# Performance work log

Hardware: AMD Instinct MI355X
Metric: run time of the kernel (lower is better)

## Reference

```python
import jax, jax.numpy as jnp
import numpy as np

N = 100000
E = 1600000
IN, HID, OUT = 128, 256, 47


def _glorot(key, shape):
    fan_in, fan_out = shape
    lim = np.sqrt(6.0 / (fan_in + fan_out))
    return jax.random.uniform(key, shape, jnp.float32, -lim, lim)


def setup_inputs() -> dict:
    key = jax.random.key(0)
    ks = jax.random.split(key, 12)
    x = jax.random.normal(ks[0], (N, IN), jnp.float32)
    src = jax.random.randint(ks[1], (E,), 0, N, jnp.int32)
    dst = jax.random.randint(ks[2], (E,), 0, N, jnp.int32)
    dims = [(IN, HID), (HID, HID), (HID, OUT)]
    inp = {"x": x, "src": src, "dst": dst}
    for i, (di, do) in enumerate(dims, 1):
        inp[f"w_self{i}"] = _glorot(ks[2 + 3 * i - 2], (di, do))
        inp[f"w_neigh{i}"] = _glorot(ks[2 + 3 * i - 1], (di, do))
        inp[f"b{i}"] = jnp.zeros((do,), jnp.float32)
    return inp


def sage_conv(x, src, dst, w_self, w_neigh, b):
    n = x.shape[0]
    msg = x[src]                                              # [E, d] gather
    summed = jax.ops.segment_sum(msg, dst, num_segments=n)    # [N, d]
    deg = jax.ops.segment_sum(jnp.ones((src.shape[0],), x.dtype), dst, num_segments=n)
    h_neigh = summed / jnp.maximum(deg, 1.0)[:, None]         # mean aggregate
    return x @ w_self + h_neigh @ w_neigh + b


def reference(x, src, dst, w_self1, w_neigh1, b1, w_self2, w_neigh2, b2, w_self3, w_neigh3, b3):
    h = sage_conv(x, src, dst, w_self1, w_neigh1, b1)
    h = jax.nn.relu(h)  # dropout = identity in eval mode
    h = sage_conv(h, src, dst, w_self2, w_neigh2, b2)
    h = jax.nn.relu(h)
    h = sage_conv(h, src, dst, w_self3, w_neigh3, b3)
    return h
```

## Files before the change

kernel.cpp:

```cpp
#include <hip/hip_runtime.h>

#define N_NODES 100000
#define N_EDGES 1600000

typedef __attribute__((ext_vector_type(8))) _Float16 half8;
typedef __attribute__((ext_vector_type(4))) _Float16 half4v;
typedef __attribute__((ext_vector_type(4))) float floatx4;


__global__ void deg_rank(const int* __restrict__ dst, int* __restrict__ deg,
                         int* __restrict__ rank, int e) {
    int i = blockIdx.x * blockDim.x + threadIdx.x;
    if (i < e) rank[i] = atomicAdd(&deg[dst[i]], 1);
}


__global__ __launch_bounds__(256) void scan_partial(const int* __restrict__ deg,
                                                    int* __restrict__ bsum, int n) {
    __shared__ int wsum[4];
    int t = threadIdx.x;
    int base = blockIdx.x * 2048 + t * 8;
    int tsum = 0;
    #pragma unroll
    for (int k = 0; k < 8; ++k) {
        int idx = base + k;
        tsum += (idx < n) ? deg[idx] : 0;
    }
    #pragma unroll
    for (int d = 1; d < 64; d <<= 1) tsum += __shfl_xor(tsum, d, 64);
    if ((t & 63) == 0) wsum[t >> 6] = tsum;
    __syncthreads();
    if (t == 0) bsum[blockIdx.x] = wsum[0] + wsum[1] + wsum[2] + wsum[3];
}

__global__ void scan_blocksums(const int* __restrict__ bsum, int* __restrict__ bbase, int nb) {
    int t = threadIdx.x;
    int v = (t < nb) ? bsum[t] : 0;
    int s = v;
    #pragma unroll
    for (int d = 1; d < 64; d <<= 1) {
        int u = __shfl_up(s, d, 64);
        if (t >= d) s += u;
    }
    if (t < nb) bbase[t] = s - v;
    if (t == 63) bbase[nb] = s;
}

__global__ __launch_bounds__(256) void scan_write(const int* __restrict__ deg,
                                                  const int* __restrict__ bbase,
                                                  int* __restrict__ offs, int n, int nb) {
    __shared__ int wsum[4];
    int t = threadIdx.x;
    int lane = t & 63, w = t >> 6;
    int base = blockIdx.x * 2048 + t * 8;
    int v[8];
    #pragma unroll
    for (int k = 0; k < 8; ++k) {
        int idx = base + k;
        v[k] = (idx < n) ? deg[idx] : 0;
    }
    int tsum = 0;
    #pragma unroll
    for (int k = 0; k < 8; ++k) { int x = v[k]; v[k] = tsum; tsum += x; }
    int s = tsum;
    #pragma unroll
    for (int d = 1; d < 64; d <<= 1) {
        int u = __shfl_up(s, d, 64);
        if (lane >= d) s += u;
    }
    if (lane == 63) wsum[w] = s;
    __syncthreads();
    int wb = 0;
    for (int j = 0; j < w; ++j) wb += wsum[j];
    int texcl = bbase[blockIdx.x] + wb + (s - tsum);
    #pragma unroll
    for (int k = 0; k < 8; ++k) {
        int idx = base + k;
        if (idx < n) offs[idx] = texcl + v[k];
    }
    if (blockIdx.x == 0 && t == 0) offs[n] = bbase[nb];
}

__global__ void fill_csr2(const int* __restrict__ src, const int* __restrict__ dst,
                          const int* __restrict__ offs, const int* __restrict__ rank,
                          int* __restrict__ csr, int e) {
    int i = blockIdx.x * blockDim.x + threadIdx.x;
    if (i < e) csr[offs[dst[i]] + rank[i]] = src[i];
}


__global__ void cvt_f16(const float4* __restrict__ in, half4v* __restrict__ oh, int n4) {
    int i = blockIdx.x * blockDim.x + threadIdx.x;
    if (i >= n4) return;
    float4 v = in[i];
    half4v h;
    h[0] = (_Float16)v.x; h[1] = (_Float16)v.y;
    h[2] = (_Float16)v.z; h[3] = (_Float16)v.w;
    oh[i] = h;
}


__global__ void prep_all(const float* __restrict__ ws1, const float* __restrict__ wn1,
                         const float* __restrict__ ws2, const float* __restrict__ wn2,
                         const float* __restrict__ ws3, const float* __restrict__ wn3,
                         _Float16* __restrict__ o1s, _Float16* __restrict__ o1n,
                         _Float16* __restrict__ o2s, _Float16* __restrict__ o2n,
                         _Float16* __restrict__ o3c) {
    int i = blockIdx.x * blockDim.x + threadIdx.x;
    if (i < 65536) {
        const float* W = (i < 32768) ? ws1 : wn1;
        _Float16* O = (i < 32768) ? o1s : o1n;
        int j = i & 32767;
        int nn = j >> 7, k = j & 127;
        O[j] = (_Float16)W[k * 256 + nn];
    } else if (i < 196608) {
        int j = i - 65536;
        const float* W = (j < 65536) ? ws2 : wn2;
        _Float16* O = (j < 65536) ? o2s : o2n;
        j &= 65535;
        int nn = j >> 8, k = j & 255;
        O[j] = (_Float16)W[k * 256 + nn];
    } else if (i < 221184) {
        int j = i - 196608;
        const float* W = (j < 12288) ? ws3 : wn3;
        _Float16* O = o3c + ((j < 12288) ? 0 : 12288);
        j = (j < 12288) ? j : j - 12288;
        int nn = j >> 8, k = j & 255;
        O[j] = (nn < 47) ? (_Float16)W[k * 47 + nn] : (_Float16)0.f;
    }
}


__global__ __launch_bounds__(256) void aggP(const _Float16* __restrict__ Xp,
                                            const int* __restrict__ csr,
                                            const int* __restrict__ offs,
                                            _Float16* __restrict__ Pp, int n) {
    int node = blockIdx.x * 4 + (threadIdx.x >> 6);
    int lane = threadIdx.x & 63;
    int qtr = lane >> 4;
    int sl = lane & 15;
    if (node >= n) return;
    int e0 = offs[node], e1 = offs[node + 1];
    float a[8] = {0.f, 0.f, 0.f, 0.f, 0.f, 0.f, 0.f, 0.f};
    int e = e0;
    for (; e + 16 <= e1; e += 16) {
        int s0 = csr[e + qtr];
        int s1 = csr[e + 4 + qtr];
        int s2 = csr[e + 8 + qtr];
        int s3 = csr[e + 12 + qtr];
        half8 u0 = ((const half8*)(Xp + (size_t)s0 * 128))[sl];
        half8 u1 = ((const half8*)(Xp + (size_t)s1 * 128))[sl];
        half8 u2 = ((const half8*)(Xp + (size_t)s2 * 128))[sl];
        half8 u3 = ((const half8*)(Xp + (size_t)s3 * 128))[sl];
        #pragma unroll
        for (int j = 0; j < 8; ++j) a[j] += (float)u0[j];
        #pragma unroll
        for (int j = 0; j < 8; ++j) a[j] += (float)u1[j];
        #pragma unroll
        for (int j = 0; j < 8; ++j) a[j] += (float)u2[j];
        #pragma unroll
        for (int j = 0; j < 8; ++j) a[j] += (float)u3[j];
    }
    for (; e + 8 <= e1; e += 8) {
        int s0 = csr[e + qtr];
        int s1 = csr[e + 4 + qtr];
        half8 u0 = ((const half8*)(Xp + (size_t)s0 * 128))[sl];
        half8 u1 = ((const half8*)(Xp + (size_t)s1 * 128))[sl];
        #pragma unroll
        for (int j = 0; j < 8; ++j) a[j] += (float)u0[j];
        #pragma unroll
        for (int j = 0; j < 8; ++j) a[j] += (float)u1[j];
    }
    for (; e + 4 <= e1; e += 4) {
        int s = csr[e + qtr];
        half8 u = ((const half8*)(Xp + (size_t)s * 128))[sl];
        #pragma unroll
        for (int j = 0; j < 8; ++j) a[j] += (float)u[j];
    }
    int rem = e1 - e;
    if (qtr < rem) {
        int s = csr[e + qtr];
        half8 u = ((const half8*)(Xp + (size_t)s * 128))[sl];
        #pragma unroll
        for (int j = 0; j < 8; ++j) a[j] += (float)u[j];
    }
    #pragma unroll
    for (int j = 0; j < 8; ++j) {
        a[j] += __shfl_xor(a[j], 16);
        a[j] += __shfl_xor(a[j], 32);
    }
    if (lane < 16) {
        float inv = 1.0f / fmaxf((float)(e1 - e0), 1.0f);
        half8 rh;
        #pragma unroll
        for (int j = 0; j < 8; ++j) rh[j] = (_Float16)(a[j] * inv);
        ((half8*)(Pp + (size_t)node * 128))[sl] = rh;
    }
}

__global__ __launch_bounds__(256) void agg_l3(const _Float16* __restrict__ Y,
                                              const float* __restrict__ S,
                                              const int* __restrict__ csr,
                                              const int* __restrict__ offs,
                                              float* __restrict__ out, int n) {
    int node = blockIdx.x * 4 + (threadIdx.x >> 6);
    int lane = threadIdx.x & 63;
    int qtr = lane >> 4;
    int sl = lane & 15;
    int c = sl < 12 ? sl : 11;
    if (node >= n) return;
    int e0 = offs[node], e1 = offs[node + 1];
    float a0 = 0.f, a1 = 0.f, a2 = 0.f, a3 = 0.f;
    int e = e0;
    for (; e + 8 <= e1; e += 8) {
        int s0 = csr[e + qtr];
        int s1 = csr[e + 4 + qtr];
        half4v f0 = ((const half4v*)(Y + (size_t)s0 * 48))[c];
        half4v f1 = ((const half4v*)(Y + (size_t)s1 * 48))[c];
        a0 += (float)f0[0] + (float)f1[0];
        a1 += (float)f0[1] + (float)f1[1];
        a2 += (float)f0[2] + (float)f1[2];
        a3 += (float)f0[3] + (float)f1[3];
    }
    for (; e + 4 <= e1; e += 4) {
        int s = csr[e + qtr];
        half4v f = ((const half4v*)(Y + (size_t)s * 48))[c];
        a0 += (float)f[0]; a1 += (float)f[1]; a2 += (float)f[2]; a3 += (float)f[3];
    }
    int rem = e1 - e;
    if (qtr < rem) {
        int s = csr[e + qtr];
        half4v f = ((const half4v*)(Y + (size_t)s * 48))[c];
        a0 += (float)f[0]; a1 += (float)f[1]; a2 += (float)f[2]; a3 += (float)f[3];
    }
    a0 += __shfl_xor(a0, 16); a0 += __shfl_xor(a0, 32);
    a1 += __shfl_xor(a1, 16); a1 += __shfl_xor(a1, 32);
    a2 += __shfl_xor(a2, 16); a2 += __shfl_xor(a2, 32);
    a3 += __shfl_xor(a3, 16); a3 += __shfl_xor(a3, 32);
    if (lane < 12) {
        float inv = 1.0f / fmaxf((float)(e1 - e0), 1.0f);
        float4 sv = ((const float4*)(S + (size_t)node * 48))[c];
        float r[4] = {sv.x + a0 * inv, sv.y + a1 * inv, sv.z + a2 * inv, sv.w + a3 * inv};
        #pragma unroll
        for (int k = 0; k < 4; ++k) {
            int col = c * 4 + k;
            if (col < 47) out[(size_t)node * 47 + col] = r[k];
        }
    }
}


template <int NTILES, int OUTFMT>
__global__ __launch_bounds__(256, 2) void gemm_mfma(
    const _Float16* __restrict__ A1h, const _Float16* __restrict__ A2h,
    const _Float16* __restrict__ W1, const _Float16* __restrict__ W2,
    const float* __restrict__ bias, float* __restrict__ outS, _Float16* __restrict__ outY,
    _Float16* __restrict__ outh, int n, int K, int dout, int relu, int phases) {
    constexpr int NPAD = NTILES * 16;
    constexpr int LDT = 36;
    __shared__ _Float16 Bs[NPAD * LDT];

    const int t = threadIdx.x;
    const int bm = blockIdx.x * 128;
    const int lane = t & 63;
    const int w = t >> 6;
    const int quad = lane >> 4;
    const int tl = lane & 15;
    const int r0 = bm + w * 32 + tl;
    const int r1 = r0 + 16;
    const size_t PS = (size_t)n * 128;

    floatx4 acc[2][NTILES];
    #pragma unroll
    for (int i = 0; i < 2; ++i)
        #pragma unroll
        for (int j = 0; j < NTILES; ++j) acc[i][j] = (floatx4){0.f, 0.f, 0.f, 0.f};

    const int spp = K >> 5;
    const int nsteps = phases * spp;

    half8 pb0, pb1, pb2, pb3;
    half8 pah0 = {0}, pah1 = {0};

    if (t < NPAD) {
        const half8* p = (const half8*)(W1 + (size_t)t * K);
        pb0 = p[0]; pb1 = p[1]; pb2 = p[2]; pb3 = p[3];
    }
    {
        int kq = quad * 8;
        if (r0 < n) pah0 = *(const half8*)(A1h + (size_t)r0 * 128 + kq);
        if (r1 < n) pah1 = *(const half8*)(A1h + (size_t)r1 * 128 + kq);
    }

    for (int s = 0; s < nsteps; ++s) {
        __syncthreads();
        if (t < NPAD) {
            *(half8*)&Bs[t * LDT + 0]  = pb0;
            *(half8*)&Bs[t * LDT + 8]  = pb1;
            *(half8*)&Bs[t * LDT + 16] = pb2;
            *(half8*)&Bs[t * LDT + 24] = pb3;
        }
        __syncthreads();
        half8 ah0 = pah0, ah1 = pah1;
        if (s + 1 < nsteps) {
            int s2 = s + 1;
            int ph2 = (s2 >= spp) ? 1 : 0;
            int k02 = (ph2 ? s2 - spp : s2) << 5;
            if (t < NPAD) {
                const _Float16* W = ph2 ? W2 : W1;
                const half8* p = (const half8*)(W + (size_t)t * K + k02);
                pb0 = p[0]; pb1 = p[1]; pb2 = p[2]; pb3 = p[3];
            }
            const _Float16* Ah = ph2 ? A2h : A1h;
            int kq = k02 + quad * 8;
            const _Float16* Ab = Ah + ((kq >> 7) ? PS : (size_t)0) + (kq & 127);
            pah0 = (half8){0}; pah1 = (half8){0};
            if (r0 < n) pah0 = *(const half8*)(Ab + (size_t)r0 * 128);
            if (r1 < n) pah1 = *(const half8*)(Ab + (size_t)r1 * 128);
        }
        #pragma unroll
        for (int nt = 0; nt < NTILES; ++nt) {
            half8 bh = *(const half8*)&Bs[(nt * 16 + tl) * LDT + quad * 8];
            acc[0][nt] = __builtin_amdgcn_mfma_f32_16x16x32_f16(ah0, bh, acc[0][nt], 0, 0, 0);
            acc[1][nt] = __builtin_amdgcn_mfma_f32_16x16x32_f16(ah1, bh, acc[1][nt], 0, 0, 0);
        }
    }

    #pragma unroll
    for (int mt = 0; mt < 2; ++mt) {
        #pragma unroll
        for (int nt = 0; nt < NTILES; ++nt) {
            int gc = nt * 16 + tl;
            if (OUTFMT == 1 && gc >= dout) continue;
            #pragma unroll
            for (int r = 0; r < 4; ++r) {
                int gr = bm + w * 32 + mt * 16 + quad * 4 + r;
                if (gr >= n) continue;
                float v = acc[mt][nt][r];
                if (OUTFMT == 1) {
                    v += bias[gc];
                    if (relu) v = fmaxf(v, 0.f);
                    outh[(size_t)(gc >> 7) * PS + (size_t)gr * 128 + (gc & 127)] = (_Float16)v;
                } else {
                    if (gc < 48) {
                        v += (gc < 47) ? bias[gc] : 0.f;
                        outS[(size_t)gr * 48 + gc] = v;
                    } else {
                        outY[(size_t)gr * 48 + (gc - 48)] = (_Float16)v;
                    }
                }
            }
        }
    }
}

extern "C" void kernel_launch(void* const* d_in, const int* in_sizes, int n_in,
                              void* d_out, int out_size, void* d_ws, size_t ws_size,
                              hipStream_t stream) {
    (void)in_sizes; (void)n_in; (void)out_size; (void)ws_size;
    const int N = N_NODES, E = N_EDGES;
    const float* x = (const float*)d_in[0];
    const int* src = (const int*)d_in[1];
    const int* dst = (const int*)d_in[2];
    const float* w_self1 = (const float*)d_in[3];
    const float* w_neigh1 = (const float*)d_in[4];
    const float* b1 = (const float*)d_in[5];
    const float* w_self2 = (const float*)d_in[6];
    const float* w_neigh2 = (const float*)d_in[7];
    const float* b2 = (const float*)d_in[8];
    const float* w_self3 = (const float*)d_in[9];
    const float* w_neigh3 = (const float*)d_in[10];
    const float* b3 = (const float*)d_in[11];
    float* out = (float*)d_out;

    _Float16* Ph = (_Float16*)d_ws;
    _Float16* Hh = Ph + (size_t)N * 256;
    int* deg = (int*)(Hh + (size_t)N * 256);
    int* offs = deg + N;
    int* csr = offs + N + 4;
    _Float16* wbuf = (_Float16*)(csr + E);
    _Float16* w1s = wbuf;
    _Float16* w1n = w1s + 32768;
    _Float16* w2s = w1n + 32768;
    _Float16* w2n = w2s + 65536;
    _Float16* w3c = w2n + 65536;
    int* bsum = (int*)(w3c + 24576);
    int* bbase = bsum + 64;
    int* rank = (int*)Ph;
    _Float16* xh = Ph + (size_t)N * 128;
    float* S = (float*)Ph;
    _Float16* Y = (_Float16*)(S + (size_t)N * 48);

    const int NB = (N + 2047) / 2048;

    hipMemsetAsync(deg, 0, N * sizeof(int), stream);
    deg_rank<<<(E + 255) / 256, 256, 0, stream>>>(dst, deg, rank, E);
    scan_partial<<<NB, 256, 0, stream>>>(deg, bsum, N);
    scan_blocksums<<<1, 64, 0, stream>>>(bsum, bbase, NB);
    scan_write<<<NB, 256, 0, stream>>>(deg, bbase, offs, N, NB);
    fill_csr2<<<(E + 255) / 256, 256, 0, stream>>>(src, dst, offs, rank, csr, E);

    cvt_f16<<<(N * 128 / 4 + 255) / 256, 256, 0, stream>>>((const float4*)x, (half4v*)xh,
                                                           N * 128 / 4);
    prep_all<<<(221184 + 255) / 256, 256, 0, stream>>>(w_self1, w_neigh1, w_self2, w_neigh2,
                                                       w_self3, w_neigh3, w1s, w1n, w2s, w2n,
                                                       w3c);

    int gemmGrid = (N + 127) / 128;
    int aggGrid = (N + 3) / 4;

    aggP<<<aggGrid, 256, 0, stream>>>(xh, csr, offs, Ph, N);
    gemm_mfma<16, 1><<<gemmGrid, 256, 0, stream>>>(xh, Ph, w1s, w1n, b1, nullptr, nullptr,
                                                   Hh, N, 128, 256, 1, 2);
    aggP<<<aggGrid, 256, 0, stream>>>(Hh, csr, offs, Ph, N);
    aggP<<<aggGrid, 256, 0, stream>>>(Hh + (size_t)N * 128, csr, offs, Ph + (size_t)N * 128, N);
    gemm_mfma<16, 1><<<gemmGrid, 256, 0, stream>>>(Hh, Ph, w2s, w2n, b2, nullptr, nullptr,
                                                   Hh, N, 256, 256, 1, 2);
    gemm_mfma<6, 2><<<gemmGrid, 256, 0, stream>>>(Hh, nullptr, w3c, nullptr, b3, S, Y,
                                                  nullptr, N, 256, 96, 0, 1);
    agg_l3<<<aggGrid, 256, 0, stream>>>(Y, S, csr, offs, out, N);
}
```

Measured before the change: 641.5 us.

## Load GEMM weights directly from global into registers and double-buffer A loads

Removes the shared-memory staging of weight tiles and both per-step __syncthreads in the MFMA GEMM. Each wave now reads its B fragments straight from global memory, relying on L1/L2 caching of the small weight matrices. A-operand prefetch moves to a two-deep register pipeline with the loop unrolled by two. This trades barrier and LDS traffic for redundant global/cache reads of the weights across waves, plus higher register pressure. The unroll also assumes nsteps is even.

```diff
diff --git a/kernel.cpp b/kernel.cpp
--- a/kernel.cpp
+++ b/kernel.cpp
@@ -256,10 +256,6 @@
     const _Float16* __restrict__ W1, const _Float16* __restrict__ W2,
     const float* __restrict__ bias, float* __restrict__ outS, _Float16* __restrict__ outY,
     _Float16* __restrict__ outh, int n, int K, int dout, int relu, int phases) {
-    constexpr int NPAD = NTILES * 16;
-    constexpr int LDT = 36;
-    __shared__ _Float16 Bs[NPAD * LDT];
-
     const int t = threadIdx.x;
     const int bm = blockIdx.x * 128;
     const int lane = t & 63;
@@ -279,50 +275,55 @@
     const int spp = K >> 5;
     const int nsteps = phases * spp;
 
-    half8 pb0, pb1, pb2, pb3;
-    half8 pah0 = {0}, pah1 = {0};
-
-    if (t < NPAD) {
-        const half8* p = (const half8*)(W1 + (size_t)t * K);
-        pb0 = p[0]; pb1 = p[1]; pb2 = p[2]; pb3 = p[3];
-    }
-    {
-        int kq = quad * 8;
-        if (r0 < n) pah0 = *(const half8*)(A1h + (size_t)r0 * 128 + kq);
-        if (r1 < n) pah1 = *(const half8*)(A1h + (size_t)r1 * 128 + kq);
-    }
-
-    for (int s = 0; s < nsteps; ++s) {
-        __syncthreads();
-        if (t < NPAD) {
-            *(half8*)&Bs[t * LDT + 0]  = pb0;
-            *(half8*)&Bs[t * LDT + 8]  = pb1;
-            *(half8*)&Bs[t * LDT + 16] = pb2;
-            *(half8*)&Bs[t * LDT + 24] = pb3;
+    half8 a0A = {0}, a1A = {0}, a0B = {0}, a1B = {0};
+
+    auto aload = [&](int s2, half8& d0, half8& d1) {
+        int ph2 = (s2 >= spp) ? 1 : 0;
+        int k02 = (ph2 ? s2 - spp : s2) << 5;
+        const _Float16* Ah = ph2 ? A2h : A1h;
+        int kq = k02 + quad * 8;
+        const _Float16* Ab = Ah + ((kq >> 7) ? PS : (size_t)0) + (kq & 127);
+        d0 = (half8){0}; d1 = (half8){0};
+        if (r0 < n) d0 = *(const half8*)(Ab + (size_t)r0 * 128);
+        if (r1 < n) d1 = *(const half8*)(Ab + (size_t)r1 * 128);
+    };
+
+    aload(0, a0A, a1A);
+    aload(1, a0B, a1B);
+
+    for (int s = 0; s < nsteps; s += 2) {
+        {
+            int ph2 = (s >= spp) ? 1 : 0;
+            int k02 = (ph2 ? s - spp : s) << 5;
+            const _Float16* Wb = (ph2 ? W2 : W1) + (size_t)tl * K + k02 + quad * 8;
+            half8 bh[NTILES];
+            #pragma unroll
+            for (int nt = 0; nt < NTILES; ++nt)
+                bh[nt] = *(const half8*)(Wb + (size_t)(nt * 16) * K);
+            half8 ca0 = a0A, ca1 = a1A;
+            if (s + 2 < nsteps) aload(s + 2, a0A, a1A);
+            #pragma unroll
+            for (int nt = 0; nt < NTILES; ++nt) {
+                acc[0][nt] = __builtin_amdgcn_mfma_f32_16x16x32_f16(ca0, bh[nt], acc[0][nt], 0, 0, 0);
+                acc[1][nt] = __builtin_amdgcn_mfma_f32_16x16x32_f16(ca1, bh[nt], acc[1][nt], 0, 0, 0);
+            }
         }
-        __syncthreads();
-        half8 ah0 = pah0, ah1 = pah1;
-        if (s + 1 < nsteps) {
-            int s2 = s + 1;
-            int ph2 = (s2 >= spp) ? 1 : 0;
-            int k02 = (ph2 ? s2 - spp : s2) << 5;
-            if (t < NPAD) {
-                const _Float16* W = ph2 ? W2 : W1;
-                const half8* p = (const half8*)(W + (size_t)t * K + k02);
-                pb0 = p[0]; pb1 = p[1]; pb2 = p[2]; pb3 = p[3];
+        {
+            int s1 = s + 1;
+            int ph2 = (s1 >= spp) ? 1 : 0;
+            int k02 = (ph2 ? s1 - spp : s1) << 5;
+            const _Float16* Wb = (ph2 ? W2 : W1) + (size_t)tl * K + k02 + quad * 8;
+            half8 bh[NTILES];
+            #pragma unroll
+            for (int nt = 0; nt < NTILES; ++nt)
+                bh[nt] = *(const half8*)(Wb + (size_t)(nt * 16) * K);
+            half8 ca0 = a0B, ca1 = a1B;
+            if (s1 + 2 < nsteps) aload(s1 + 2, a0B, a1B);
+            #pragma unroll
+            for (int nt = 0; nt < NTILES; ++nt) {
+                acc[0][nt] = __builtin_amdgcn_mfma_f32_16x16x32_f16(ca0, bh[nt], acc[0][nt], 0, 0, 0);
+                acc[1][nt] = __builtin_amdgcn_mfma_f32_16x16x32_f16(ca1, bh[nt], acc[1][nt], 0, 0, 0);
             }
-            const _Float16* Ah = ph2 ? A2h : A1h;
-            int kq = k02 + quad * 8;
-            const _Float16* Ab = Ah + ((kq >> 7) ? PS : (size_t)0) + (kq & 127);
-            pah0 = (half8){0}; pah1 = (half8){0};
-            if (r0 < n) pah0 = *(const half8*)(Ab + (size_t)r0 * 128);
-            if (r1 < n) pah1 = *(const half8*)(Ab + (size_t)r1 * 128);
-        }
-        #pragma unroll
-        for (int nt = 0; nt < NTILES; ++nt) {
-            half8 bh = *(const half8*)&Bs[(nt * 16 + tl) * LDT + quad * 8];
-            acc[0][nt] = __builtin_amdgcn_mfma_f32_16x16x32_f16(ah0, bh, acc[0][nt], 0, 0, 0);
-            acc[1][nt] = __builtin_amdgcn_mfma_f32_16x16x32_f16(ah1, bh, acc[1][nt], 0, 0, 0);
         }
     }
 
```

New measurement: 755.5 us. 1.18x slower.
